# Performance work log

Measured on AMD Instinct MI355X. Metric: run time of the kernel, lower is better.

The kernel has to match this reference:

```python
import jax, jax.numpy as jnp
import numpy as np

M1, M2 = 32, 32  # max_modes1, max_modes2
C_IN, C_OUT = 64, 64


def _neg_k(a):
    # torch.roll(torch.flip(a, dims=[-2,-1]), shifts=(1,1), dims=[-2,-1])
    return jnp.roll(jnp.flip(a, axis=(-2, -1)), shift=(1, 1), axis=(-2, -1))


def compl_mul2d(x1, x2):
    x1n = _neg_k(x1)
    x2n = _neg_k(x2)
    e = lambda a, b: jnp.einsum('bixy,ioxy->boxy', a, b)
    return 0.5 * (e(x1, x2) - e(x1n, x2n) + e(x1, x2n) + e(x1n, x2))


def setup_inputs() -> dict:
    key = jax.random.key(0)
    k1, k2, k3 = jax.random.split(key, 3)
    scale = 1.0 / (C_IN * C_OUT)
    return {
        "x": jax.random.normal(k1, (16, C_IN, 256, 256), dtype=jnp.float32),
        "weights1_re": scale * jax.random.uniform(k2, (C_IN, C_OUT, M1, M2), dtype=jnp.float32),
        "weights1_im": scale * jax.random.uniform(k3, (C_IN, C_OUT, M1, M2), dtype=jnp.float32),
        "error_estimate": 1,  # must be >= 1: smaller modes would break the einsum vs full weights
    }


def reference(x, weights1_re, weights1_im, error_estimate):
    B, Ci, H, W = x.shape
    modes1 = min(M1, max(1, int(M1 * error_estimate)))
    modes2 = min(M2, max(1, int(M2 * error_estimate)))
    weights1 = jax.lax.complex(weights1_re, weights1_im)  # complex64

    # spectral branch (computed exactly as in the original; note the original
    # module never uses out_ft in its return value)
    x_ft = jnp.fft.rfftn(x, axes=(2, 3))  # [B, Ci, H, W//2+1] complex64
    block = compl_mul2d(x_ft[:, :, :modes1, :modes2], weights1)
    out_ft = jnp.zeros((B, C_OUT, H, W // 2 + 1), dtype=jnp.complex64)
    out_ft = out_ft.at[:, :, :modes1, :modes2].set(block)

    # idht(x) with dim=None: fftn over ALL axes, (real+imag)/numel
    X = jnp.fft.fftn(x, axes=(0, 1, 2, 3))
    out = (X.real + X.imag) / x.size
    return out.astype(jnp.float32)
```

## Files before the change

kernel.cpp:

```cpp
#include <hip/hip_runtime.h>


#define NB 16
#define NC 64
#define NH 256
#define NW 256
#define WP 132
#define CSTRIDE (NH*WP)
#define BSTRIDE (NC*NH*WP)

__device__ __forceinline__ float2 cadd(float2 a, float2 b){ return make_float2(a.x+b.x, a.y+b.y); }
__device__ __forceinline__ float2 csub(float2 a, float2 b){ return make_float2(a.x-b.x, a.y-b.y); }
__device__ __forceinline__ float2 cmul(float2 a, float2 b){ return make_float2(a.x*b.x - a.y*b.y, a.x*b.y + a.y*b.x); }

__device__ __forceinline__ float2 twd(float frac){
  float sn, cs;
  __sincosf(-6.28318530717958647692f * frac, &sn, &cs);
  return make_float2(cs, sn);
}

__device__ __forceinline__ void dft4(float2&a,float2&b,float2&c,float2&d){
  float2 t0=cadd(a,c), t1=csub(a,c), t2=cadd(b,d), t3=csub(b,d);
  float2 t3i = make_float2(t3.y, -t3.x);
  a=cadd(t0,t2); c=csub(t0,t2); b=cadd(t1,t3i); d=csub(t1,t3i);
}

__device__ __forceinline__ void fft8(float2 v[8]){
  float2 e0=v[0],e1=v[2],e2=v[4],e3=v[6];
  float2 o0=v[1],o1=v[3],o2=v[5],o3=v[7];
  dft4(e0,e1,e2,e3); dft4(o0,o1,o2,o3);
  const float s=0.70710678118654752440f;
  float2 w1o=make_float2(s*(o1.x+o1.y), s*(o1.y-o1.x));
  float2 w2o=make_float2(o2.y, -o2.x);
  float2 w3o=make_float2(s*(o3.y-o3.x), -s*(o3.x+o3.y));
  v[0]=cadd(e0,o0); v[4]=csub(e0,o0);
  v[1]=cadd(e1,w1o); v[5]=csub(e1,w1o);
  v[2]=cadd(e2,w2o); v[6]=csub(e2,w2o);
  v[3]=cadd(e3,w3o); v[7]=csub(e3,w3o);
}

__device__ __forceinline__ void fft16(float2 v[16]){
  float2 e[8], o[8];
#pragma unroll
  for(int i=0;i<8;i++){ e[i]=v[2*i]; o[i]=v[2*i+1]; }
  fft8(e); fft8(o);
  const float c1=0.92387953251128675613f, s1=0.38268343236508977173f, s=0.70710678118654752440f;
  const float wr[8] = {1.f,  c1,  s,  s1, 0.f, -s1, -s, -c1};
  const float wi[8] = {0.f, -s1, -s, -c1, -1.f, -c1, -s, -s1};
#pragma unroll
  for(int k=0;k<8;k++){
    float2 wo = make_float2(wr[k]*o[k].x - wi[k]*o[k].y, wr[k]*o[k].y + wi[k]*o[k].x);
    v[k]=cadd(e[k],wo); v[k+8]=csub(e[k],wo);
  }
}

__global__ __launch_bounds__(256) void k1_fftW(const float* __restrict__ x, float2* __restrict__ S){
  __shared__ float2 lds[16][16][17];
  const int j    = threadIdx.x & 15;
  const int line = threadIdx.x >> 4;
  const int gline = blockIdx.x * 16 + line;
  const float* px = x + (size_t)gline * NW;
  float2 v[16];
#pragma unroll
  for(int n1=0;n1<16;n1++) v[n1] = make_float2(px[16*n1 + j], 0.f);
  fft16(v);
#pragma unroll
  for(int k1=0;k1<16;k1++){
    v[k1] = cmul(v[k1], twd((float)(j*k1) * (1.0f/256.0f)));
    lds[line][k1][j] = v[k1];
  }
  __syncthreads();
  float2 u[16];
#pragma unroll
  for(int n2=0;n2<16;n2++) u[n2] = lds[line][j][n2];
  fft16(u);
  float2* ps = S + (size_t)gline * WP;
#pragma unroll
  for(int k2=0;k2<8;k2++) ps[j + 16*k2] = u[k2];
  if(j==0) ps[128] = u[8];
}

__global__ __launch_bounds__(256) void k2_fftH(float2* __restrict__ S){
  __shared__ float2 lds[16][16][17];
  const int kwo  = threadIdx.x & 15;
  const int j    = threadIdx.x >> 4;
  const int tile = blockIdx.x % 9;
  const int slice= blockIdx.x / 9;
  const int kw   = tile*16 + kwo;
  const bool act = (kw <= 128);
  float2* base = S + (size_t)slice * NH * WP + kw;
  float2 v[16];
#pragma unroll
  for(int n1=0;n1<16;n1++) v[n1] = act ? base[(16*n1 + j) * WP] : make_float2(0.f,0.f);
  fft16(v);
#pragma unroll
  for(int k1=0;k1<16;k1++){
    v[k1] = cmul(v[k1], twd((float)(j*k1) * (1.0f/256.0f)));
    lds[kwo][k1][j] = v[k1];
  }
  __syncthreads();
  float2 u[16];
#pragma unroll
  for(int n2=0;n2<16;n2++) u[n2] = lds[kwo][j][n2];
  fft16(u);
  if(act){
#pragma unroll
    for(int k2=0;k2<16;k2++) base[(j + 16*k2) * WP] = u[k2];
  }
}

__global__ __launch_bounds__(256) void k3_fftC(float2* __restrict__ S){
  __shared__ float2 lds[32][8][9];
  const int kwo  = threadIdx.x & 31;
  const int j    = threadIdx.x >> 5;
  const int tile = blockIdx.x % 5;
  const int bh   = blockIdx.x / 5;
  const int b = bh >> 8, h = bh & 255;
  const int kw = tile*32 + kwo;
  const bool act = (kw <= 128);
  float2* base = S + (size_t)b * BSTRIDE + (size_t)h * WP + kw;
  float2 v[8];
#pragma unroll
  for(int n1=0;n1<8;n1++) v[n1] = act ? base[(8*n1 + j) * CSTRIDE] : make_float2(0.f,0.f);
  fft8(v);
#pragma unroll
  for(int k1=0;k1<8;k1++){
    v[k1] = cmul(v[k1], twd((float)(j*k1) * (1.0f/64.0f)));
    lds[kwo][k1][j] = v[k1];
  }
  __syncthreads();
  float2 u[8];
#pragma unroll
  for(int n2=0;n2<8;n2++) u[n2] = lds[kwo][j][n2];
  fft8(u);
  if(act){
#pragma unroll
    for(int k2=0;k2<8;k2++) base[(j + 8*k2) * CSTRIDE] = u[k2];
  }
}

__global__ __launch_bounds__(256) void k4_fftB(float2* __restrict__ S){
  const int idx = blockIdx.x * 256 + threadIdx.x;
  const int kw = idx % WP;
  const int hc = idx / WP;
  const int h = hc & 255, c = hc >> 8;
  if(kw > 128 || c >= NC) return;
  float2* base = S + (size_t)c * CSTRIDE + (size_t)h * WP + kw;
  float2 v[16];
#pragma unroll
  for(int b=0;b<16;b++) v[b] = base[(size_t)b * BSTRIDE];
  fft16(v);
#pragma unroll
  for(int b=0;b<16;b++) base[(size_t)b * BSTRIDE] = v[b];
}

__global__ __launch_bounds__(256) void k5_final(const float2* __restrict__ S, float* __restrict__ out){
  const int idx = blockIdx.x * 256 + threadIdx.x;
  const int w = idx & 255;
  const int h = (idx >> 8) & 255;
  const int c = (idx >> 16) & 63;
  const int b = idx >> 22;
  const float inv = 1.0f / 67108864.0f;
  float val;
  if(w <= 128){
    float2 z = S[((size_t)(b*NC + c) * NH + h) * WP + w];
    val = (z.x + z.y) * inv;
  } else {
    const int p  = 256 - w;
    const int b2 = (16 - b) & 15;
    const int c2 = (64 - c) & 63;
    const int h2 = (256 - h) & 255;
    float2 z = S[((size_t)(b2*NC + c2) * NH + h2) * WP + p];
    val = (z.x - z.y) * inv;
  }
  out[idx] = val;
}

extern "C" void kernel_launch(void* const* d_in, const int* in_sizes, int n_in,
                              void* d_out, int out_size, void* d_ws, size_t ws_size,
                              hipStream_t stream) {
  const float* x = (const float*)d_in[0];
  float* out = (float*)d_out;
  float2* S  = (float2*)d_ws;

  k1_fftW<<<NB*NC*NH/16, 256, 0, stream>>>(x, S);
  k2_fftH<<<NB*NC*9,     256, 0, stream>>>(S);
  k3_fftC<<<NB*NH*5,     256, 0, stream>>>(S);
  k4_fftB<<<(NC*NH*WP+255)/256, 256, 0, stream>>>(S);
  k5_final<<<(NB*NC*NH*NW)/256, 256, 0, stream>>>(S, out);
}
```

Measured before the change: 963.4 us.

## Fuse channel FFT, batch FFT and Hermitian output into one LDS-tiled kernel

Replaces the separate channel-axis FFT, batch-axis FFT and final output kernels with one kernel. Each block loads an (h, 8-column) slab covering all batches and channels into LDS, runs the 64-point and 16-point transforms there, and writes both the direct and Hermitian-mirrored outputs straight to the result. This removes two full read/write passes over the spectrum buffer and the scattered gather in the output step. In exchange each block uses a large LDS tile, which lowers occupancy, and the mirrored output stores are scattered.

```diff
diff --git a/kernel.cpp b/kernel.cpp
--- a/kernel.cpp
+++ b/kernel.cpp
@@ -8,6 +8,7 @@
 #define WP 132
 #define CSTRIDE (NH*WP)
 #define BSTRIDE (NC*NH*WP)
+#define LSTRIDE (NH*WP)
 
 __device__ __forceinline__ float2 cadd(float2 a, float2 b){ return make_float2(a.x+b.x, a.y+b.y); }
 __device__ __forceinline__ float2 csub(float2 a, float2 b){ return make_float2(a.x-b.x, a.y-b.y); }
@@ -109,71 +110,88 @@
   }
 }
 
-__global__ __launch_bounds__(256) void k3_fftC(float2* __restrict__ S){
-  __shared__ float2 lds[32][8][9];
-  const int kwo  = threadIdx.x & 31;
-  const int j    = threadIdx.x >> 5;
-  const int tile = blockIdx.x % 5;
-  const int bh   = blockIdx.x / 5;
-  const int b = bh >> 8, h = bh & 255;
-  const int kw = tile*32 + kwo;
-  const bool act = (kw <= 128);
-  float2* base = S + (size_t)b * BSTRIDE + (size_t)h * WP + kw;
-  float2 v[8];
-#pragma unroll
-  for(int n1=0;n1<8;n1++) v[n1] = act ? base[(8*n1 + j) * CSTRIDE] : make_float2(0.f,0.f);
-  fft8(v);
-#pragma unroll
-  for(int k1=0;k1<8;k1++){
-    v[k1] = cmul(v[k1], twd((float)(j*k1) * (1.0f/64.0f)));
-    lds[kwo][k1][j] = v[k1];
-  }
-  __syncthreads();
-  float2 u[8];
-#pragma unroll
-  for(int n2=0;n2<8;n2++) u[n2] = lds[kwo][j][n2];
-  fft8(u);
-  if(act){
-#pragma unroll
-    for(int k2=0;k2<8;k2++) base[(j + 8*k2) * CSTRIDE] = u[k2];
-  }
-}
-
-__global__ __launch_bounds__(256) void k4_fftB(float2* __restrict__ S){
-  const int idx = blockIdx.x * 256 + threadIdx.x;
-  const int kw = idx % WP;
-  const int hc = idx / WP;
-  const int h = hc & 255, c = hc >> 8;
-  if(kw > 128 || c >= NC) return;
-  float2* base = S + (size_t)c * CSTRIDE + (size_t)h * WP + kw;
-  float2 v[16];
-#pragma unroll
-  for(int b=0;b<16;b++) v[b] = base[(size_t)b * BSTRIDE];
-  fft16(v);
-#pragma unroll
-  for(int b=0;b<16;b++) base[(size_t)b * BSTRIDE] = v[b];
-}
-
-__global__ __launch_bounds__(256) void k5_final(const float2* __restrict__ S, float* __restrict__ out){
-  const int idx = blockIdx.x * 256 + threadIdx.x;
-  const int w = idx & 255;
-  const int h = (idx >> 8) & 255;
-  const int c = (idx >> 16) & 63;
-  const int b = idx >> 22;
+__global__ __launch_bounds__(256) void k3_fused(const float2* __restrict__ S, float* __restrict__ out){
+  __shared__ float2 A[1024][9];
+  const int t    = threadIdx.x;
+  const int h    = blockIdx.x & 255;
+  const int tile = blockIdx.x >> 8;
+  const int kw0  = tile * 8;
+  const float2* Sbase = S + (size_t)h * WP + kw0;
+
+#pragma unroll
+  for(int r=0;r<16;r++){
+    int f    = t + 256*r;
+    int line = f >> 2;
+    int part = f & 3;
+    float4 val;
+    if(kw0 + part*2 + 1 < WP){
+      val = *(const float4*)(Sbase + (size_t)line * LSTRIDE + part*2);
+    } else {
+      val = make_float4(0.f,0.f,0.f,0.f);
+    }
+    A[line][part*2]     = make_float2(val.x, val.y);
+    A[line][part*2 + 1] = make_float2(val.z, val.w);
+  }
+  __syncthreads();
+
+#pragma unroll
+  for(int q=0;q<4;q++){
+    int item = t + 256*q;
+    int kwo = item & 7, n2 = (item>>3) & 7, b = item >> 6;
+    float2 v[8];
+#pragma unroll
+    for(int n1=0;n1<8;n1++) v[n1] = A[b*64 + 8*n1 + n2][kwo];
+    fft8(v);
+#pragma unroll
+    for(int k1=0;k1<8;k1++) A[b*64 + 8*k1 + n2][kwo] = cmul(v[k1], twd((float)(n2*k1) * (1.0f/64.0f)));
+  }
+  __syncthreads();
+
+  {
+    float2 u[4][8];
+#pragma unroll
+    for(int q=0;q<4;q++){
+      int item = t + 256*q;
+      int kwo = item & 7, k1 = (item>>3) & 7, b = item >> 6;
+#pragma unroll
+      for(int n2=0;n2<8;n2++) u[q][n2] = A[b*64 + 8*k1 + n2][kwo];
+      fft8(u[q]);
+    }
+    __syncthreads();
+#pragma unroll
+    for(int q=0;q<4;q++){
+      int item = t + 256*q;
+      int kwo = item & 7, k1 = (item>>3) & 7, b = item >> 6;
+#pragma unroll
+      for(int k2=0;k2<8;k2++) A[b*64 + (k1 + 8*k2)][kwo] = u[q][k2];
+    }
+  }
+  __syncthreads();
+
   const float inv = 1.0f / 67108864.0f;
-  float val;
-  if(w <= 128){
-    float2 z = S[((size_t)(b*NC + c) * NH + h) * WP + w];
-    val = (z.x + z.y) * inv;
-  } else {
-    const int p  = 256 - w;
-    const int b2 = (16 - b) & 15;
-    const int c2 = (64 - c) & 63;
-    const int h2 = (256 - h) & 255;
-    float2 z = S[((size_t)(b2*NC + c2) * NH + h2) * WP + p];
-    val = (z.x - z.y) * inv;
-  }
-  out[idx] = val;
+  const int h2 = (NH - h) & 255;
+#pragma unroll
+  for(int q=0;q<2;q++){
+    int item = t + 256*q;
+    int kwo = item & 7, kc = item >> 3;
+    float2 v[16];
+#pragma unroll
+    for(int b=0;b<16;b++) v[b] = A[b*64 + kc][kwo];
+    fft16(v);
+    const int kw = kw0 + kwo;
+    if(kw <= 128){
+      const int kc2 = (NC - kc) & 63;
+#pragma unroll
+      for(int kb=0;kb<16;kb++){
+        float2 z = v[kb];
+        out[(((size_t)kb*NC + kc)*NH + h)*NW + kw] = (z.x + z.y) * inv;
+        if(kw >= 1 && kw <= 127){
+          const int kb2 = (16 - kb) & 15;
+          out[(((size_t)kb2*NC + kc2)*NH + h2)*NW + (NW - kw)] = (z.x - z.y) * inv;
+        }
+      }
+    }
+  }
 }
 
 extern "C" void kernel_launch(void* const* d_in, const int* in_sizes, int n_in,
@@ -185,7 +203,5 @@
 
   k1_fftW<<<NB*NC*NH/16, 256, 0, stream>>>(x, S);
   k2_fftH<<<NB*NC*9,     256, 0, stream>>>(S);
-  k3_fftC<<<NB*NH*5,     256, 0, stream>>>(S);
-  k4_fftB<<<(NC*NH*WP+255)/256, 256, 0, stream>>>(S);
-  k5_final<<<(NB*NC*NH*NW)/256, 256, 0, stream>>>(S, out);
-}
+  k3_fused<<<17*256,     256, 0, stream>>>(S, out);
+}
```

Result: faster. 909.1 us (-5.6%).
